# Kernel optimization log

Measured on AMD Instinct MI355X. Metric: run time of the kernel, lower is better.

Reference implementation:

```python
import jax, jax.numpy as jnp
import numpy as np

N, D, G, H, M = 500000, 128, 64, 128, 256  # bag size, local_dim, global_dim, attn_hidden, mlp_hidden
TEMP = 1.0


def setup_inputs() -> dict:
    key = jax.random.key(0)
    ks = jax.random.split(key, 8)
    s = 0.05
    return {
        "bag": jax.random.normal(ks[0], (N, D), jnp.float32),
        "global_feat": jax.random.normal(ks[1], (G,), jnp.float32),
        # attention_V: Linear(D, H) + Tanh
        "Wv": jax.random.normal(ks[2], (H, D), jnp.float32) * s,
        "bv": jnp.zeros((H,), jnp.float32),
        # attention_U: Linear(D, H) + Sigmoid
        "Wu": jax.random.normal(ks[3], (H, D), jnp.float32) * s,
        "bu": jnp.zeros((H,), jnp.float32),
        # attention_weights: Linear(H, 1)
        "Ww": jax.random.normal(ks[4], (1, H), jnp.float32) * s,
        "bw": jnp.zeros((1,), jnp.float32),
        "W1": jax.random.normal(ks[5], (M, D + G), jnp.float32) * s,
        "b1": jnp.zeros((M,), jnp.float32),
        "W2": jax.random.normal(ks[6], (1, M), jnp.float32) * s,
        "b2": jnp.zeros((1,), jnp.float32),
    }


def reference(bag, global_feat, Wv, bv, Wu, bu, Ww, bw, W1, b1, W2, b2):
    # feature_extractor = Identity (use_feature_extractor=False); dropout = identity (eval)
    V = jnp.tanh(bag @ Wv.T + bv)            # [N, H]
    U = jax.nn.sigmoid(bag @ Wu.T + bu)      # [N, H]
    Ggate = V * U                            # [N, H]
    A_raw = Ggate @ Ww.T + bw                # [N, 1]
    alpha = jax.nn.softmax(A_raw / TEMP, axis=0)  # softmax over bag dim
    bag_embedding = alpha.T @ bag            # [1, D]
    fused = jnp.concatenate([bag_embedding, global_feat.reshape(1, -1)], axis=1)  # [1, D+G]
    h = jax.nn.leaky_relu(fused @ W1.T + b1, negative_slope=0.01)  # [1, M]
    score = h @ W2.T + b2                    # [1, 1]
    return (score, alpha)
```

## Files before the change

### kernel.cpp

```cpp
#include <hip/hip_runtime.h>
#include <hip/hip_bf16.h>

#define N_BAG 500000
#define DIM   128
#define ROWS_PER_ITER 64
#define ITERS 8
#define ROWS_PER_BLOCK 512
#define NBLK  977
#define GDIM  64
#define LDB   136

typedef __attribute__((ext_vector_type(8))) __bf16 bf16x8;
typedef __attribute__((ext_vector_type(4))) __bf16 bf16x4;
typedef __attribute__((ext_vector_type(4))) float  f32x4;

union BF8 { bf16x8 v; __bf16 e[8]; };

__device__ __forceinline__ float fast_rcp(float x) { return __builtin_amdgcn_rcpf(x); }

__global__ __launch_bounds__(256, 3)
void attn_pass1(const float* __restrict__ bag,
                const float* __restrict__ Wv, const float* __restrict__ bv,
                const float* __restrict__ Wu, const float* __restrict__ bu,
                const float* __restrict__ Ww, const float* __restrict__ bw,
                float* __restrict__ aOut,
                float* __restrict__ blkM, float* __restrict__ blkS,
                float* __restrict__ blkW)
{
    __shared__ __align__(16) __bf16 Xs[2][ROWS_PER_ITER][LDB];
    __shared__ float a_part[4][ROWS_PER_ITER];
    __shared__ float fin[256][4];

    const int tid = threadIdx.x;
    const int w   = tid >> 6;
    const int L   = tid & 63;
    const int m16 = L & 15;
    const int q   = L >> 4;
    const int hh  = L >> 5;
    const int c32 = L & 31;
    const int blk = blockIdx.x;
    const int rowBase = blk * ROWS_PER_BLOCK;

    BF8 fv[2][4], fu[2][4];
    float bvv[2], buu[2], www[2];
#pragma unroll
    for (int ht = 0; ht < 2; ++ht) {
        const int h = w*32 + ht*16 + m16;
        bvv[ht] = bv[h]; buu[ht] = bu[h]; www[ht] = Ww[h];
#pragma unroll
        for (int s = 0; s < 4; ++s) {
            const int d0 = s*32 + q*8;
            const float4 v0 = *(const float4*)(Wv + h*DIM + d0);
            const float4 v1 = *(const float4*)(Wv + h*DIM + d0 + 4);
            const float4 u0 = *(const float4*)(Wu + h*DIM + d0);
            const float4 u1 = *(const float4*)(Wu + h*DIM + d0 + 4);
            fv[ht][s].e[0]=(__bf16)v0.x; fv[ht][s].e[1]=(__bf16)v0.y;
            fv[ht][s].e[2]=(__bf16)v0.z; fv[ht][s].e[3]=(__bf16)v0.w;
            fv[ht][s].e[4]=(__bf16)v1.x; fv[ht][s].e[5]=(__bf16)v1.y;
            fv[ht][s].e[6]=(__bf16)v1.z; fv[ht][s].e[7]=(__bf16)v1.w;
            fu[ht][s].e[0]=(__bf16)u0.x; fu[ht][s].e[1]=(__bf16)u0.y;
            fu[ht][s].e[2]=(__bf16)u0.z; fu[ht][s].e[3]=(__bf16)u0.w;
            fu[ht][s].e[4]=(__bf16)u1.x; fu[ht][s].e[5]=(__bf16)u1.y;
            fu[ht][s].e[6]=(__bf16)u1.z; fu[ht][s].e[7]=(__bf16)u1.w;
        }
    }
    const float bw0 = bw[0];

    float4 stg[8];
    {
#pragma unroll
        for (int i = 0; i < 8; ++i) {
            int r = rowBase + i*8 + w*2 + hh;
            if (r >= N_BAG) r = N_BAG - 1;
            stg[i] = *(const float4*)(bag + (size_t)r*DIM + c32*4);
        }
    }

    float m_run = -1e30f, s_run = 0.0f;
    float wacc0 = 0.f, wacc1 = 0.f, wacc2 = 0.f, wacc3 = 0.f;

    for (int it = 0; it < ITERS; ++it) {
        const int buf = it & 1;
        const int tileStart = rowBase + it*ROWS_PER_ITER;

#pragma unroll
        for (int i = 0; i < 8; ++i) {
            const int row = i*8 + w*2 + hh;
            bf16x4 pk;
            pk.x = (__bf16)stg[i].x; pk.y = (__bf16)stg[i].y;
            pk.z = (__bf16)stg[i].z; pk.w = (__bf16)stg[i].w;
            *(bf16x4*)&Xs[buf][row][c32*4] = pk;
        }
        __syncthreads();

        if (it + 1 < ITERS) {
            const int ts2 = tileStart + ROWS_PER_ITER;
#pragma unroll
            for (int i = 0; i < 8; ++i) {
                int r = ts2 + i*8 + w*2 + hh;
                if (r >= N_BAG) r = N_BAG - 1;
                stg[i] = *(const float4*)(bag + (size_t)r*DIM + c32*4);
            }
        }

#pragma unroll
        for (int r = 0; r < 4; ++r) {
            bf16x8 af[4];
#pragma unroll
            for (int s = 0; s < 4; ++s)
                af[s] = *(const bf16x8*)&Xs[buf][r*16 + m16][s*32 + q*8];
            f32x4 accV[2], accU[2];
#pragma unroll
            for (int ht = 0; ht < 2; ++ht) {
                accV[ht] = (f32x4){0.f,0.f,0.f,0.f};
                accU[ht] = (f32x4){0.f,0.f,0.f,0.f};
            }
#pragma unroll
            for (int s = 0; s < 4; ++s) {
#pragma unroll
                for (int ht = 0; ht < 2; ++ht) {
                    accV[ht] = __builtin_amdgcn_mfma_f32_16x16x32_bf16(af[s], fv[ht][s].v, accV[ht], 0, 0, 0);
                    accU[ht] = __builtin_amdgcn_mfma_f32_16x16x32_bf16(af[s], fu[ht][s].v, accU[ht], 0, 0, 0);
                }
            }
            float psum[4];
#pragma unroll
            for (int g = 0; g < 4; ++g) {
                float p = 0.0f;
#pragma unroll
                for (int ht = 0; ht < 2; ++ht) {
                    const float z = accV[ht][g] + bvv[ht];
                    const float y = accU[ht][g] + buu[ht];
                    const float tv = 2.0f * fast_rcp(1.0f + __expf(-2.0f*z)) - 1.0f;
                    const float su = fast_rcp(1.0f + __expf(-y));
                    p += tv * su * www[ht];
                }
                p += __shfl_xor(p, 1); p += __shfl_xor(p, 2);
                p += __shfl_xor(p, 4); p += __shfl_xor(p, 8);
                psum[g] = p;
            }
            if (m16 == 0)
                *(float4*)&a_part[w][r*16 + q*4] = make_float4(psum[0], psum[1], psum[2], psum[3]);
        }
        __syncthreads();

        float a = a_part[0][L] + a_part[1][L] + a_part[2][L] + a_part[3][L] + bw0;
        const int grow = tileStart + L;
        if (grow >= N_BAG) a = -1e30f;
        else if (w == 0)   aOut[grow] = a;

        float mt = a;
        mt = fmaxf(mt, __shfl_xor(mt, 1));  mt = fmaxf(mt, __shfl_xor(mt, 2));
        mt = fmaxf(mt, __shfl_xor(mt, 4));  mt = fmaxf(mt, __shfl_xor(mt, 8));
        mt = fmaxf(mt, __shfl_xor(mt, 16)); mt = fmaxf(mt, __shfl_xor(mt, 32));
        const float mnew = fmaxf(m_run, mt);
        const float sc   = __expf(m_run - mnew);
        const float e    = __expf(a - mnew);
        m_run = mnew;
        float es = e;
        es += __shfl_xor(es, 1);  es += __shfl_xor(es, 2);
        es += __shfl_xor(es, 4);  es += __shfl_xor(es, 8);
        es += __shfl_xor(es, 16); es += __shfl_xor(es, 32);
        s_run = s_run * sc + es;

        float s0 = 0.f, s1 = 0.f, s2 = 0.f, s3 = 0.f;
#pragma unroll
        for (int i = 0; i < 8; ++i) {
            const int row = i*8 + w*2 + hh;
            const float ei = __shfl(e, row);
            const bf16x4 xb = *(const bf16x4*)&Xs[buf][row][c32*4];
            s0 += ei * (float)xb.x; s1 += ei * (float)xb.y;
            s2 += ei * (float)xb.z; s3 += ei * (float)xb.w;
        }
        wacc0 = wacc0*sc + s0; wacc1 = wacc1*sc + s1;
        wacc2 = wacc2*sc + s2; wacc3 = wacc3*sc + s3;
    }

    fin[tid][0] = wacc0; fin[tid][1] = wacc1;
    fin[tid][2] = wacc2; fin[tid][3] = wacc3;
    __syncthreads();
    if (tid < 128) {
        float v = 0.0f;
#pragma unroll
        for (int k = 0; k < 8; ++k) {
            const int t = (k >> 1)*64 + (k & 1)*32 + (tid >> 2);
            v += fin[t][tid & 3];
        }
        blkW[blk*DIM + tid] = v;
    }
    if (tid == 0) { blkM[blk] = m_run; blkS[blk] = s_run; }
}

__global__ void head_kernel(const float* __restrict__ blkM, const float* __restrict__ blkS,
                            const float* __restrict__ blkW, const float* __restrict__ gfeat,
                            const float* __restrict__ W1, const float* __restrict__ b1,
                            const float* __restrict__ W2, const float* __restrict__ b2,
                            float* __restrict__ out, float* __restrict__ ms)
{
    __shared__ float red[1024];
    __shared__ float scale_s[1024];
    __shared__ float f[192];
    __shared__ float hbuf[256];
    const int tid = threadIdx.x;

    red[tid] = (tid < NBLK) ? blkM[tid] : -1e30f;
    __syncthreads();
    for (int s = 512; s > 0; s >>= 1) {
        if (tid < s) red[tid] = fmaxf(red[tid], red[tid + s]);
        __syncthreads();
    }
    const float M = red[0]; __syncthreads();

    float sc = 0.0f, ls = 0.0f;
    if (tid < NBLK) { sc = __expf(blkM[tid] - M); ls = blkS[tid] * sc; }
    scale_s[tid] = sc;
    red[tid] = ls; __syncthreads();
    for (int s = 512; s > 0; s >>= 1) {
        if (tid < s) red[tid] += red[tid + s];
        __syncthreads();
    }
    const float S = red[0]; __syncthreads();

    const int c = tid & 127, g = tid >> 7;
    float acc = 0.0f;
    for (int b = g; b < NBLK; b += 8) acc += blkW[b*DIM + c] * scale_s[b];
    red[tid] = acc; __syncthreads();
    if (tid < 128) {
        float E = 0.0f;
#pragma unroll
        for (int g2 = 0; g2 < 8; ++g2) E += red[g2*128 + tid];
        f[tid] = E / S;
    }
    if (tid >= 128 && tid < 128 + GDIM) f[tid] = gfeat[tid - 128];
    if (tid == 0) { ms[0] = M; ms[1] = 1.0f / S; }
    __syncthreads();

    if (tid < 256) {
        float a2 = b1[tid];
        const float4* w1p = (const float4*)(W1 + tid * (DIM + GDIM));
        const float4* fp  = (const float4*)f;
#pragma unroll 4
        for (int k = 0; k < (DIM + GDIM) / 4; ++k) {
            const float4 a4 = w1p[k]; const float4 f4 = fp[k];
            a2 += a4.x*f4.x + a4.y*f4.y + a4.z*f4.z + a4.w*f4.w;
        }
        hbuf[tid] = a2 > 0.0f ? a2 : 0.01f * a2;
    }
    __syncthreads();

    red[tid] = (tid < 256) ? hbuf[tid] * W2[tid] : 0.0f;
    __syncthreads();
    for (int s = 512; s > 0; s >>= 1) {
        if (tid < s) red[tid] += red[tid + s];
        __syncthreads();
    }
    if (tid == 0) out[0] = red[0] + b2[0];
}

__global__ void alpha_kernel(float* __restrict__ alpha, const float* __restrict__ ms)
{
    const int i = blockIdx.x * blockDim.x + threadIdx.x;
    const float M = ms[0], invS = ms[1];
    if (i < N_BAG) alpha[i] = __expf(alpha[i] - M) * invS;
}

extern "C" void kernel_launch(void* const* d_in, const int* in_sizes, int n_in,
                              void* d_out, int out_size, void* d_ws, size_t ws_size,
                              hipStream_t stream)
{
    const float* bag   = (const float*)d_in[0];
    const float* gfeat = (const float*)d_in[1];
    const float* Wv    = (const float*)d_in[2];
    const float* bv    = (const float*)d_in[3];
    const float* Wu    = (const float*)d_in[4];
    const float* bu    = (const float*)d_in[5];
    const float* Ww    = (const float*)d_in[6];
    const float* bw    = (const float*)d_in[7];
    const float* W1    = (const float*)d_in[8];
    const float* b1    = (const float*)d_in[9];
    const float* W2    = (const float*)d_in[10];
    const float* b2    = (const float*)d_in[11];
    float* out = (float*)d_out;
    float* ws  = (float*)d_ws;

    float* blkM = ws;
    float* blkS = ws + 1024;
    float* blkW = ws + 2048;
    float* msv  = ws + 2048 + 125056;

    attn_pass1<<<NBLK, 256, 0, stream>>>(bag, Wv, bv, Wu, bu, Ww, bw,
                                         out + 1, blkM, blkS, blkW);
    head_kernel<<<1, 1024, 0, stream>>>(blkM, blkS, blkW, gfeat, W1, b1, W2, b2,
                                        out, msv);
    alpha_kernel<<<(N_BAG + 255) / 256, 256, 0, stream>>>(out + 1, msv);
}
```

Baseline: 431.1 us.

## Halve tile rows, alias LDS, raise occupancy, split head into parallel kernels

The main attention kernel now handles 32 rows per iteration over 16 iterations, loads A fragments per k-step instead of all at once, and reuses the LDS tile buffer for the final reduction scratch. Together with launch bounds of 4 blocks per CU, this aims to cut register and LDS pressure so more waves run and hide memory latency. The single-block head kernel is split into three kernels, with a 64-block atomic reduction over per-block embeddings replacing the serial one. In exchange, half the lanes sit idle in the softmax step, there are more barriers per row, and there are two extra kernel launches.

After: 432.0 us. Within noise of the previous version (+0.2%).

```diff
diff --git a/kernel.cpp b/kernel.cpp
--- a/kernel.cpp
+++ b/kernel.cpp
@@ -3,8 +3,8 @@
 
 #define N_BAG 500000
 #define DIM   128
-#define ROWS_PER_ITER 64
-#define ITERS 8
+#define ROWS_PER_ITER 32
+#define ITERS 16
 #define ROWS_PER_BLOCK 512
 #define NBLK  977
 #define GDIM  64
@@ -18,7 +18,7 @@
 
 __device__ __forceinline__ float fast_rcp(float x) { return __builtin_amdgcn_rcpf(x); }
 
-__global__ __launch_bounds__(256, 3)
+__global__ __launch_bounds__(256, 4)
 void attn_pass1(const float* __restrict__ bag,
                 const float* __restrict__ Wv, const float* __restrict__ bv,
                 const float* __restrict__ Wu, const float* __restrict__ bu,
@@ -27,9 +27,12 @@
                 float* __restrict__ blkM, float* __restrict__ blkS,
                 float* __restrict__ blkW)
 {
-    __shared__ __align__(16) __bf16 Xs[2][ROWS_PER_ITER][LDB];
+    __shared__ __align__(16) unsigned char smem[2 * ROWS_PER_ITER * LDB * 2];
     __shared__ float a_part[4][ROWS_PER_ITER];
-    __shared__ float fin[256][4];
+
+    typedef __bf16 XsRow[ROWS_PER_ITER][LDB];
+    XsRow* Xs = (XsRow*)smem;
+    float (*fin)[4] = (float(*)[4])smem;
 
     const int tid = threadIdx.x;
     const int w   = tid >> 6;
@@ -66,14 +69,12 @@
     }
     const float bw0 = bw[0];
 
-    float4 stg[8];
-    {
-#pragma unroll
-        for (int i = 0; i < 8; ++i) {
-            int r = rowBase + i*8 + w*2 + hh;
-            if (r >= N_BAG) r = N_BAG - 1;
-            stg[i] = *(const float4*)(bag + (size_t)r*DIM + c32*4);
-        }
+    float4 stg[4];
+#pragma unroll
+    for (int i = 0; i < 4; ++i) {
+        int r = rowBase + i*8 + w*2 + hh;
+        if (r >= N_BAG) r = N_BAG - 1;
+        stg[i] = *(const float4*)(bag + (size_t)r*DIM + c32*4);
     }
 
     float m_run = -1e30f, s_run = 0.0f;
@@ -84,7 +85,7 @@
         const int tileStart = rowBase + it*ROWS_PER_ITER;
 
 #pragma unroll
-        for (int i = 0; i < 8; ++i) {
+        for (int i = 0; i < 4; ++i) {
             const int row = i*8 + w*2 + hh;
             bf16x4 pk;
             pk.x = (__bf16)stg[i].x; pk.y = (__bf16)stg[i].y;
@@ -96,7 +97,7 @@
         if (it + 1 < ITERS) {
             const int ts2 = tileStart + ROWS_PER_ITER;
 #pragma unroll
-            for (int i = 0; i < 8; ++i) {
+            for (int i = 0; i < 4; ++i) {
                 int r = ts2 + i*8 + w*2 + hh;
                 if (r >= N_BAG) r = N_BAG - 1;
                 stg[i] = *(const float4*)(bag + (size_t)r*DIM + c32*4);
@@ -104,11 +105,7 @@
         }
 
 #pragma unroll
-        for (int r = 0; r < 4; ++r) {
-            bf16x8 af[4];
-#pragma unroll
-            for (int s = 0; s < 4; ++s)
-                af[s] = *(const bf16x8*)&Xs[buf][r*16 + m16][s*32 + q*8];
+        for (int r = 0; r < 2; ++r) {
             f32x4 accV[2], accU[2];
 #pragma unroll
             for (int ht = 0; ht < 2; ++ht) {
@@ -117,10 +114,11 @@
             }
 #pragma unroll
             for (int s = 0; s < 4; ++s) {
+                const bf16x8 af = *(const bf16x8*)&Xs[buf][r*16 + m16][s*32 + q*8];
 #pragma unroll
                 for (int ht = 0; ht < 2; ++ht) {
-                    accV[ht] = __builtin_amdgcn_mfma_f32_16x16x32_bf16(af[s], fv[ht][s].v, accV[ht], 0, 0, 0);
-                    accU[ht] = __builtin_amdgcn_mfma_f32_16x16x32_bf16(af[s], fu[ht][s].v, accU[ht], 0, 0, 0);
+                    accV[ht] = __builtin_amdgcn_mfma_f32_16x16x32_bf16(af, fv[ht][s].v, accV[ht], 0, 0, 0);
+                    accU[ht] = __builtin_amdgcn_mfma_f32_16x16x32_bf16(af, fu[ht][s].v, accU[ht], 0, 0, 0);
                 }
             }
             float psum[4];
@@ -144,10 +142,11 @@
         }
         __syncthreads();
 
-        float a = a_part[0][L] + a_part[1][L] + a_part[2][L] + a_part[3][L] + bw0;
-        const int grow = tileStart + L;
-        if (grow >= N_BAG) a = -1e30f;
-        else if (w == 0)   aOut[grow] = a;
+        const int li = L & 31;
+        float a = a_part[0][li] + a_part[1][li] + a_part[2][li] + a_part[3][li] + bw0;
+        const int grow = tileStart + li;
+        if (L >= 32 || grow >= N_BAG) a = -1e30f;
+        else if (w == 0)              aOut[grow] = a;
 
         float mt = a;
         mt = fmaxf(mt, __shfl_xor(mt, 1));  mt = fmaxf(mt, __shfl_xor(mt, 2));
@@ -165,7 +164,7 @@
 
         float s0 = 0.f, s1 = 0.f, s2 = 0.f, s3 = 0.f;
 #pragma unroll
-        for (int i = 0; i < 8; ++i) {
+        for (int i = 0; i < 4; ++i) {
             const int row = i*8 + w*2 + hh;
             const float ei = __shfl(e, row);
             const bf16x4 xb = *(const bf16x4*)&Xs[buf][row][c32*4];
@@ -176,6 +175,7 @@
         wacc2 = wacc2*sc + s2; wacc3 = wacc3*sc + s3;
     }
 
+    __syncthreads();
     fin[tid][0] = wacc0; fin[tid][1] = wacc1;
     fin[tid][2] = wacc2; fin[tid][3] = wacc3;
     __syncthreads();
@@ -191,16 +191,11 @@
     if (tid == 0) { blkM[blk] = m_run; blkS[blk] = s_run; }
 }
 
-__global__ void head_kernel(const float* __restrict__ blkM, const float* __restrict__ blkS,
-                            const float* __restrict__ blkW, const float* __restrict__ gfeat,
-                            const float* __restrict__ W1, const float* __restrict__ b1,
-                            const float* __restrict__ W2, const float* __restrict__ b2,
-                            float* __restrict__ out, float* __restrict__ ms)
+__global__ void head1(const float* __restrict__ blkM, const float* __restrict__ blkS,
+                      float* __restrict__ scaleArr, float* __restrict__ ms,
+                      float* __restrict__ E)
 {
     __shared__ float red[1024];
-    __shared__ float scale_s[1024];
-    __shared__ float f[192];
-    __shared__ float hbuf[256];
     const int tid = threadIdx.x;
 
     red[tid] = (tid < NBLK) ? blkM[tid] : -1e30f;
@@ -212,45 +207,59 @@
     const float M = red[0]; __syncthreads();
 
     float sc = 0.0f, ls = 0.0f;
-    if (tid < NBLK) { sc = __expf(blkM[tid] - M); ls = blkS[tid] * sc; }
-    scale_s[tid] = sc;
+    if (tid < NBLK) {
+        sc = __expf(blkM[tid] - M);
+        ls = blkS[tid] * sc;
+        scaleArr[tid] = sc;
+    }
     red[tid] = ls; __syncthreads();
     for (int s = 512; s > 0; s >>= 1) {
         if (tid < s) red[tid] += red[tid + s];
         __syncthreads();
     }
-    const float S = red[0]; __syncthreads();
-
+    if (tid == 0) { ms[0] = M; ms[1] = 1.0f / red[0]; }
+    if (tid < DIM) E[tid] = 0.0f;
+}
+
+__global__ void head2(const float* __restrict__ blkW, const float* __restrict__ scaleArr,
+                      float* __restrict__ E)
+{
+    const int tid = threadIdx.x;
     const int c = tid & 127, g = tid >> 7;
     float acc = 0.0f;
-    for (int b = g; b < NBLK; b += 8) acc += blkW[b*DIM + c] * scale_s[b];
-    red[tid] = acc; __syncthreads();
-    if (tid < 128) {
-        float E = 0.0f;
-#pragma unroll
-        for (int g2 = 0; g2 < 8; ++g2) E += red[g2*128 + tid];
-        f[tid] = E / S;
-    }
-    if (tid >= 128 && tid < 128 + GDIM) f[tid] = gfeat[tid - 128];
-    if (tid == 0) { ms[0] = M; ms[1] = 1.0f / S; }
+#pragma unroll
+    for (int t = 0; t < 8; ++t) {
+        const int b = blockIdx.x*2 + g + t*128;
+        if (b < NBLK) acc += blkW[b*DIM + c] * scaleArr[b];
+    }
+    atomicAdd(&E[c], acc);
+}
+
+__global__ void head3(const float* __restrict__ E, const float* __restrict__ ms,
+                      const float* __restrict__ gfeat,
+                      const float* __restrict__ W1, const float* __restrict__ b1,
+                      const float* __restrict__ W2, const float* __restrict__ b2,
+                      float* __restrict__ out)
+{
+    __shared__ float f[DIM + GDIM];
+    __shared__ float red[256];
+    const int tid = threadIdx.x;
+
+    if (tid < DIM)                 f[tid] = E[tid] * ms[1];
+    else if (tid < DIM + GDIM)     f[tid] = gfeat[tid - DIM];
     __syncthreads();
 
-    if (tid < 256) {
-        float a2 = b1[tid];
-        const float4* w1p = (const float4*)(W1 + tid * (DIM + GDIM));
-        const float4* fp  = (const float4*)f;
+    float a2 = b1[tid];
+    const float4* w1p = (const float4*)(W1 + tid * (DIM + GDIM));
+    const float4* fp  = (const float4*)f;
 #pragma unroll 4
-        for (int k = 0; k < (DIM + GDIM) / 4; ++k) {
-            const float4 a4 = w1p[k]; const float4 f4 = fp[k];
-            a2 += a4.x*f4.x + a4.y*f4.y + a4.z*f4.z + a4.w*f4.w;
-        }
-        hbuf[tid] = a2 > 0.0f ? a2 : 0.01f * a2;
-    }
-    __syncthreads();
-
-    red[tid] = (tid < 256) ? hbuf[tid] * W2[tid] : 0.0f;
-    __syncthreads();
-    for (int s = 512; s > 0; s >>= 1) {
+    for (int k = 0; k < (DIM + GDIM) / 4; ++k) {
+        const float4 a4 = w1p[k]; const float4 f4 = fp[k];
+        a2 += a4.x*f4.x + a4.y*f4.y + a4.z*f4.z + a4.w*f4.w;
+    }
+    const float h = a2 > 0.0f ? a2 : 0.01f * a2;
+    red[tid] = h * W2[tid]; __syncthreads();
+    for (int s = 128; s > 0; s >>= 1) {
         if (tid < s) red[tid] += red[tid + s];
         __syncthreads();
     }
@@ -283,14 +292,17 @@
     float* out = (float*)d_out;
     float* ws  = (float*)d_ws;
 
-    float* blkM = ws;
-    float* blkS = ws + 1024;
-    float* blkW = ws + 2048;
-    float* msv  = ws + 2048 + 125056;
+    float* blkM     = ws;
+    float* blkS     = ws + 1024;
+    float* blkW     = ws + 2048;
+    float* msv      = ws + 2048 + 125056;
+    float* scaleArr = ws + 2048 + 125056 + 16;
+    float* Eacc     = ws + 2048 + 125056 + 16 + 1024;
 
     attn_pass1<<<NBLK, 256, 0, stream>>>(bag, Wv, bv, Wu, bu, Ww, bw,
                                          out + 1, blkM, blkS, blkW);
-    head_kernel<<<1, 1024, 0, stream>>>(blkM, blkS, blkW, gfeat, W1, b1, W2, b2,
-                                        out, msv);
+    head1<<<1, 1024, 0, stream>>>(blkM, blkS, scaleArr, msv, Eacc);
+    head2<<<64, 256, 0, stream>>>(blkW, scaleArr, Eacc);
+    head3<<<1, 256, 0, stream>>>(Eacc, msv, gfeat, W1, b1, W2, b2, out);
     alpha_kernel<<<(N_BAG + 255) / 256, 256, 0, stream>>>(out + 1, msv);
 }
```
